# Optimization experiments

Measured on AMD Instinct MI355X. Metric: run time of the kernel, lower is better.

Reference implementation:

```python
import jax, jax.numpy as jnp
import numpy as np

IN_DIM, HID, E, N = 1024, 2048, 8, 16384

def setup_inputs() -> dict:
    key = jax.random.key(0)
    ks = jax.random.split(key, 12)
    s_in = 1.0 / np.sqrt(IN_DIM)
    s_h = 1.0 / np.sqrt(HID)
    return {
        "x": jax.random.normal(ks[0], (N, IN_DIM), dtype=jnp.float32),
        "enc_W": jax.random.uniform(ks[1], (IN_DIM, HID), jnp.float32, -s_in, s_in),
        "enc_b": jax.random.uniform(ks[2], (HID,), jnp.float32, -s_in, s_in),
        "gate_W": jax.random.uniform(ks[3], (HID, E), jnp.float32, -s_h, s_h),
        "expert_W": jax.random.uniform(ks[4], (E, HID, HID), jnp.float32, -s_h, s_h),
        "expert_b": jax.random.uniform(ks[5], (E, HID), jnp.float32, -s_h, s_h),
        "res_W": jax.random.uniform(ks[6], (HID, HID), jnp.float32, -s_h, s_h),
        "res_b": jax.random.uniform(ks[7], (HID,), jnp.float32, -s_h, s_h),
        "coef_W": jax.random.uniform(ks[8], (HID, 2), jnp.float32, -s_h, s_h),
        "coef_b": jax.random.uniform(ks[9], (2,), jnp.float32, -s_h, s_h),
        "dec_W": jax.random.uniform(ks[10], (HID, IN_DIM), jnp.float32, -s_h, s_h),
        "dec_b": jax.random.uniform(ks[11], (IN_DIM,), jnp.float32, -s_h, s_h),
    }

def reference(x, enc_W, enc_b, gate_W, expert_W, expert_b, res_W, res_b, coef_W, coef_b, dec_W, dec_b):
    # Encode: Linear + ReLU -> h [N, HID]
    h = jax.nn.relu(x @ enc_W + enc_b)
    # Top-1 gating (softmax probs, argmax expert, combine weight = chosen prob)
    probs = jax.nn.softmax(h @ gate_W, axis=-1)          # [N, E]
    idx = jnp.argmax(probs, axis=-1)                     # [N]
    gate = jnp.max(probs, axis=-1, keepdims=True)        # [N, 1]
    # Dense dispatch: run every expert, select via one-hot combine
    y_all = jnp.einsum('nd,edh->neh', h, expert_W) + expert_b  # [N, E, HID]
    onehot = jax.nn.one_hot(idx, y_all.shape[1], dtype=h.dtype)
    moe_out = jnp.einsum('neh,ne->nh', y_all, onehot) * gate   # [N, HID]
    # Residual expert + learned 2-way blending coefficient
    res = h @ res_W + res_b
    coef = jax.nn.softmax(h @ coef_W + coef_b, axis=-1)        # [N, 2]
    out = moe_out * coef[:, 0:1] + res * coef[:, 1:2]
    # Decode
    return out @ dec_W + dec_b
```

## Files before the change

### kernel.cpp

```cpp
#include <hip/hip_runtime.h>


#define N_TOK 16384
#define IN_DIM 1024
#define HID 2048
#define NEXP 8
#define TAU 8.0e-3f

typedef __bf16 bf16_t;
typedef __bf16 bf16x8 __attribute__((ext_vector_type(8)));
typedef __bf16 bf16x4v __attribute__((ext_vector_type(4)));
typedef float f32x4 __attribute__((ext_vector_type(4)));
typedef unsigned short ushort_t;

#define CLAMP1E4(v) fmaxf(fminf((v), 1.0e4f), -1.0e4f)

#define ASYNC16(gp, lp)                                                        \
  __builtin_amdgcn_global_load_lds(                                            \
      (const __attribute__((address_space(1))) void*)(gp),                     \
      (__attribute__((address_space(3))) void*)(lp), 16, 0, 0)

static __device__ inline ushort_t b2u(bf16_t v) {
  union { bf16_t b; ushort_t u; } x; x.b = v; return x.u;
}

__global__ __launch_bounds__(256) void fill_bf16(bf16_t* __restrict__ p,
                                                 float v, int n) {
  const int i = blockIdx.x * 256 + threadIdx.x;
  if (i < n) p[i] = (bf16_t)v;
}

__global__ __launch_bounds__(256) void detect_dtype(
    const ushort_t* __restrict__ xr, int* __restrict__ flag) {
  __shared__ int s_bad;
  if (threadIdx.x == 0) s_bad = 0;
  __syncthreads();
  int bad = 0;
  for (int i = threadIdx.x; i < 4096; i += 256) {
    const int e = (xr[i] >> 7) & 0xFF;
    if (e >= 0xC0) bad = 1;
  }
  if (__any(bad) && (threadIdx.x & 63) == 0) atomicOr(&s_bad, 1);
  __syncthreads();
  if (threadIdx.x == 0) *flag = s_bad;
}

__global__ __launch_bounds__(256) void cvt_to_bf16_x4(
    const void* __restrict__ src, bf16_t* __restrict__ dst, int n4,
    const int* __restrict__ flagp) {
  const int f = *flagp;
  const int i = blockIdx.x * 256 + threadIdx.x;
  if (i >= n4) return;
  bf16x4v o;
  if (f) {
    const f32x4 v = ((const f32x4*)src)[i];
    o[0] = (bf16_t)v[0]; o[1] = (bf16_t)v[1];
    o[2] = (bf16_t)v[2]; o[3] = (bf16_t)v[3];
  } else {
    o = ((const bf16x4v*)src)[i];
  }
  ((bf16x4v*)dst)[i] = o;
}

__global__ __launch_bounds__(256) void cvt_small(
    const void* __restrict__ encB, const void* __restrict__ expB,
    const void* __restrict__ resB, const void* __restrict__ decB,
    const void* __restrict__ coefB, const void* __restrict__ gateW,
    const void* __restrict__ coefW, float* __restrict__ encBf,
    float* __restrict__ expBf, float* __restrict__ resBf,
    float* __restrict__ decBf, float* __restrict__ coefBf,
    bf16_t* __restrict__ gWb, bf16_t* __restrict__ cWb,
    const int* __restrict__ flagp) {
  const int f = *flagp;
  const int i = blockIdx.x * 256 + threadIdx.x;
  const int seg = blockIdx.y;
  const void* src;
  int n;
  switch (seg) {
    case 0: src = encB;  n = HID; break;
    case 1: src = expB;  n = NEXP * HID; break;
    case 2: src = resB;  n = HID; break;
    case 3: src = decB;  n = IN_DIM; break;
    case 4: src = coefB; n = 2; break;
    case 5: src = gateW; n = HID * 8; break;
    default: src = coefW; n = HID * 2; break;
  }
  if (i >= n) return;
  const float v = f ? ((const float*)src)[i] : (float)((const bf16_t*)src)[i];
  switch (seg) {
    case 0: encBf[i] = v; break;
    case 1: expBf[i] = v; break;
    case 2: resBf[i] = v; break;
    case 3: decBf[i] = v; break;
    case 4: coefBf[i] = v; break;
    case 5: gWb[i] = (bf16_t)v; break;
    default: cWb[i] = (bf16_t)v; break;
  }
}

__global__ __launch_bounds__(256) void transpose_cvt(
    const void* __restrict__ src0, ushort_t* __restrict__ dst, int R, int C,
    size_t elem_off, const int* __restrict__ flagp, size_t src_zstride,
    size_t dst_zstride) {
  __shared__ ushort_t t[32][33];
  const int f = *flagp;
  const size_t eoff = elem_off + (size_t)blockIdx.z * src_zstride;
  dst += (size_t)blockIdx.z * dst_zstride;
  const int c0 = blockIdx.x * 32, r0 = blockIdx.y * 32;
  const int tx = threadIdx.x, ty = threadIdx.y;
  if (f) {
    const float* s = (const float*)src0 + eoff;
#pragma unroll
    for (int i = 0; i < 4; ++i)
      t[ty + i * 8][tx] =
          b2u((bf16_t)s[(size_t)(r0 + ty + i * 8) * C + c0 + tx]);
  } else {
    const ushort_t* s = (const ushort_t*)src0 + eoff;
#pragma unroll
    for (int i = 0; i < 4; ++i)
      t[ty + i * 8][tx] = s[(size_t)(r0 + ty + i * 8) * C + c0 + tx];
  }
  __syncthreads();
#pragma unroll
  for (int i = 0; i < 4; ++i)
    dst[(size_t)(c0 + ty + i * 8) * R + r0 + tx] = t[tx][ty + i * 8];
}


__global__ __launch_bounds__(256) void enc_gemm(
    const bf16_t* __restrict__ A, const bf16_t* __restrict__ Bt,
    const float* __restrict__ bias, bf16_t* __restrict__ H) {
  __shared__ bf16_t As[128 * 64];
  __shared__ bf16_t Bs[128 * 64];

  const int tid = threadIdx.x, lane = tid & 63, w = tid >> 6;
  const int wr = w >> 1, wc = w & 1, quad = lane >> 4, l16 = lane & 15;
  const int m0 = blockIdx.x * 128, n0 = blockIdx.y * 128;
  const char* Ab = (const char*)A;
  const char* Bb = (const char*)Bt;
  const size_t lda = (size_t)IN_DIM * 2;

  const f32x4 fz = {0.f, 0.f, 0.f, 0.f};
  f32x4 acc[4][4];
#pragma unroll
  for (int i = 0; i < 4; ++i)
#pragma unroll
    for (int j = 0; j < 4; ++j) acc[i][j] = fz;

  size_t aoff[4], boff[4];
  int cb[4];
#pragma unroll
  for (int c = 0; c < 4; ++c) {
    cb[c] = (w * 4 + c) * 1024;
    const int o = cb[c] + lane * 16;
    const int row = o >> 7;
    const int kb = (o & 127) ^ ((row & 7) << 4);
    aoff[c] = (size_t)(m0 + row) * lda + kb;
    boff[c] = (size_t)(n0 + row) * lda + kb;
  }
  const int sw = (l16 & 7) << 3;

  for (int kt = 0; kt < IN_DIM / 64; ++kt) {
    __syncthreads();
#pragma unroll
    for (int c = 0; c < 4; ++c) {
      ASYNC16(Ab + aoff[c] + (size_t)kt * 128, (char*)As + cb[c]);
      ASYNC16(Bb + boff[c] + (size_t)kt * 128, (char*)Bs + cb[c]);
    }
    __syncthreads();

#pragma unroll
    for (int ks = 0; ks < 2; ++ks) {
      const int co = (ks * 32 + quad * 8) ^ sw;
      bf16x8 af[4], bfr[4];
#pragma unroll
      for (int i = 0; i < 4; ++i)
        af[i] = *(const bf16x8*)&As[(wr * 64 + i * 16 + l16) * 64 + co];
#pragma unroll
      for (int j = 0; j < 4; ++j)
        bfr[j] = *(const bf16x8*)&Bs[(wc * 64 + j * 16 + l16) * 64 + co];
#pragma unroll
      for (int i = 0; i < 4; ++i)
#pragma unroll
        for (int j = 0; j < 4; ++j)
          acc[i][j] = __builtin_amdgcn_mfma_f32_16x16x32_bf16(
              af[i], bfr[j], acc[i][j], 0, 0, 0);
    }
  }

  float bj[4];
  int colj[4];
#pragma unroll
  for (int j = 0; j < 4; ++j) {
    colj[j] = n0 + wc * 64 + j * 16 + l16;
    bj[j] = bias[colj[j]];
  }

#pragma unroll
  for (int i = 0; i < 4; ++i) {
#pragma unroll
    for (int r = 0; r < 4; ++r) {
      const int row = m0 + wr * 64 + i * 16 + quad * 4 + r;
#pragma unroll
      for (int j = 0; j < 4; ++j) {
        const float v = fminf(fmaxf(acc[i][j][r] + bj[j], 0.f), 1.0e4f);
        H[(size_t)row * HID + colj[j]] = (bf16_t)v;
      }
    }
  }
}

__global__ __launch_bounds__(256) void gate_from_h(
    const bf16_t* __restrict__ H, const bf16_t* __restrict__ gW,
    const bf16_t* __restrict__ cW, const float* __restrict__ coefBf,
    float* __restrict__ s0g, float* __restrict__ s1g, float* __restrict__ c0g,
    int* __restrict__ eidx, int* __restrict__ ambig, int* __restrict__ acnt,
    int* __restrict__ cnt) {
  const int tid = threadIdx.x, lane = tid & 63, w = tid >> 6;
  const int r0 = blockIdx.x * 16 + w * 4;

  float acc[4][10];
#pragma unroll
  for (int g = 0; g < 4; ++g)
#pragma unroll
    for (int o = 0; o < 10; ++o) acc[g][o] = 0.f;

#pragma unroll
  for (int it = 0; it < HID / 512; ++it) {
    const int h0 = it * 512 + lane * 8;
    bf16x8 hv[4];
#pragma unroll
    for (int g = 0; g < 4; ++g)
      hv[g] = *(const bf16x8*)(H + (size_t)(r0 + g) * HID + h0);
    const bf16_t* gp = gW + (size_t)h0 * 8;
    const bf16_t* cp = cW + (size_t)h0 * 2;
    bf16x8 cc0 = *(const bf16x8*)(cp);
    bf16x8 cc1 = *(const bf16x8*)(cp + 8);
#pragma unroll
    for (int k = 0; k < 8; ++k) {
      const bf16x8 gk = *(const bf16x8*)(gp + k * 8);
      const float ck0 = (k < 4) ? (float)cc0[(k & 3) * 2]
                                : (float)cc1[(k & 3) * 2];
      const float ck1 = (k < 4) ? (float)cc0[(k & 3) * 2 + 1]
                                : (float)cc1[(k & 3) * 2 + 1];
#pragma unroll
      for (int g = 0; g < 4; ++g) {
        const float v = (float)hv[g][k];
#pragma unroll
        for (int o = 0; o < 8; ++o) acc[g][o] += v * (float)gk[o];
        acc[g][8] += v * ck0;
        acc[g][9] += v * ck1;
      }
    }
  }

#pragma unroll
  for (int m = 1; m < 64; m <<= 1)
#pragma unroll
    for (int g = 0; g < 4; ++g)
#pragma unroll
      for (int o = 0; o < 10; ++o) acc[g][o] += __shfl_xor(acc[g][o], m);

  if (lane == 0) {
#pragma unroll
    for (int g = 0; g < 4; ++g) {
      const int r = r0 + g;
      float lv[8];
#pragma unroll
      for (int e = 0; e < 8; ++e) lv[e] = acc[g][e];
      float mx = lv[0];
      int idx = 0;
#pragma unroll
      for (int e = 1; e < 8; ++e)
        if (lv[e] > mx) { mx = lv[e]; idx = e; }
      float s2 = -1.0e30f;
#pragma unroll
      for (int e = 0; e < 8; ++e)
        if (e != idx) s2 = fmaxf(s2, lv[e]);
      float s = 0.f;
#pragma unroll
      for (int e = 0; e < 8; ++e) s += expf(lv[e] - mx);
      const float gate = 1.f / s;
      const float c0 = acc[g][8] + coefBf[0], c1 = acc[g][9] + coefBf[1];
      const float cm = fmaxf(c0, c1);
      const float e0 = expf(c0 - cm), e1 = expf(c1 - cm);
      const float inv = 1.f / (e0 + e1);
      const float p0 = e0 * inv;
      c0g[r] = p0;
      s1g[r] = e1 * inv;
      s0g[r] = gate * p0;
      eidx[r] = idx;
      atomicAdd(&cnt[idx], 1);
      if (mx - s2 < TAU) {
        const int p = atomicAdd(acnt, 1);
        ambig[p] = r;
      }
    }
  }
}

__global__ __launch_bounds__(256) void rescue_rows(
    const void* __restrict__ xraw, const void* __restrict__ encWraw,
    const float* __restrict__ encBf, const void* __restrict__ gateWraw,
    const int* __restrict__ flagp, const int* __restrict__ ambig,
    const int* __restrict__ acnt, const float* __restrict__ c0g,
    float* __restrict__ s0g, int* __restrict__ eidx, int* __restrict__ cnt) {
  const int i = blockIdx.x;
  if (i >= *acnt) return;
  const int r = ambig[i];
  const int f = *flagp;
  const int tid = threadIdx.x;

  __shared__ float xs[IN_DIM];
  if (f) {
    const float* xp = (const float*)xraw + (size_t)r * IN_DIM;
    for (int k = tid; k < IN_DIM; k += 256) xs[k] = xp[k];
  } else {
    const bf16_t* xp = (const bf16_t*)xraw + (size_t)r * IN_DIM;
    for (int k = tid; k < IN_DIM; k += 256) xs[k] = (float)xp[k];
  }
  __syncthreads();

  double hacc[8] = {0, 0, 0, 0, 0, 0, 0, 0};
  if (f) {
    const float* W = (const float*)encWraw;
    for (int k0 = 0; k0 < IN_DIM; k0 += 8) {
      float wv[8][8];
#pragma unroll
      for (int kk = 0; kk < 8; ++kk) {
        const float* Wr = W + (size_t)(k0 + kk) * HID + tid;
#pragma unroll
        for (int jj = 0; jj < 8; ++jj) wv[kk][jj] = Wr[jj * 256];
      }
#pragma unroll
      for (int kk = 0; kk < 8; ++kk) {
        const double xv = (double)xs[k0 + kk];
#pragma unroll
        for (int jj = 0; jj < 8; ++jj) hacc[jj] += xv * (double)wv[kk][jj];
      }
    }
  } else {
    const bf16_t* W = (const bf16_t*)encWraw;
    for (int k0 = 0; k0 < IN_DIM; k0 += 8) {
      float wv[8][8];
#pragma unroll
      for (int kk = 0; kk < 8; ++kk) {
        const bf16_t* Wr = W + (size_t)(k0 + kk) * HID + tid;
#pragma unroll
        for (int jj = 0; jj < 8; ++jj) wv[kk][jj] = (float)Wr[jj * 256];
      }
#pragma unroll
      for (int kk = 0; kk < 8; ++kk) {
        const double xv = (double)xs[k0 + kk];
#pragma unroll
        for (int jj = 0; jj < 8; ++jj) hacc[jj] += xv * (double)wv[kk][jj];
      }
    }
  }

  double lg[8] = {0, 0, 0, 0, 0, 0, 0, 0};
#pragma unroll
  for (int jj = 0; jj < 8; ++jj) {
    const int j = tid + jj * 256;
    double h = hacc[jj] + (double)encBf[j];
    if (h > 0.0) {
      if (f) {
        const float* g = (const float*)gateWraw + (size_t)j * 8;
#pragma unroll
        for (int e = 0; e < 8; ++e) lg[e] += h * (double)g[e];
      } else {
        const bf16_t* g = (const bf16_t*)gateWraw + (size_t)j * 8;
#pragma unroll
        for (int e = 0; e < 8; ++e) lg[e] += h * (double)(float)g[e];
      }
    }
  }
#pragma unroll
  for (int m = 1; m < 64; m <<= 1)
#pragma unroll
    for (int e = 0; e < 8; ++e) lg[e] += __shfl_xor(lg[e], m);

  __shared__ double red[4][8];
  const int w = tid >> 6, lane = tid & 63;
  if (lane == 0)
#pragma unroll
    for (int e = 0; e < 8; ++e) red[w][e] = lg[e];
  __syncthreads();
  if (tid == 0) {
    double t[8];
#pragma unroll
    for (int e = 0; e < 8; ++e)
      t[e] = red[0][e] + red[1][e] + red[2][e] + red[3][e];
    double m = t[0];
    int idx = 0;
#pragma unroll
    for (int e = 1; e < 8; ++e)
      if (t[e] > m) { m = t[e]; idx = e; }
    double s = 0.0;
#pragma unroll
    for (int e = 0; e < 8; ++e) s += exp(t[e] - m);
    s0g[r] = (float)((1.0 / s) * (double)c0g[r]);
    const int old = eidx[r];
    if (idx != old) {
      atomicSub(&cnt[old], 1);
      atomicAdd(&cnt[idx], 1);
      eidx[r] = idx;
    }
  }
}

__global__ __launch_bounds__(256) void place_rows(
    const int* __restrict__ eidx, const int* __restrict__ cnt,
    int* __restrict__ curs, int* __restrict__ permflat) {
  const int r = blockIdx.x * 256 + threadIdx.x;
  const int e = eidx[r];
  int prefix = 0;
  for (int ee = 0; ee < NEXP; ++ee)
    if (ee < e) prefix += cnt[ee];
  const int pos = atomicAdd(&curs[e], 1);
  permflat[prefix + pos] = r;
}

__global__ __launch_bounds__(256) void gather_rows(
    const bf16_t* __restrict__ H, const int* __restrict__ permflat,
    const float* __restrict__ s0g, const float* __restrict__ s1g,
    bf16_t* __restrict__ Hp, int* __restrict__ rowid,
    float* __restrict__ s0p, float* __restrict__ s1p) {
  const int w = threadIdx.x >> 6, lane = threadIdx.x & 63;
  const int p = blockIdx.x * 4 + w;
  const int r = permflat[p];
  if (lane == 0) {
    rowid[p] = r;
    s0p[p] = s0g[r];
    s1p[p] = s1g[r];
  }
  const bf16x8* src = (const bf16x8*)(H + (size_t)r * HID);
  bf16x8* dst = (bf16x8*)(Hp + (size_t)p * HID);
#pragma unroll
  for (int i = 0; i < 4; ++i) dst[lane + i * 64] = src[lane + i * 64];
}

__global__ __launch_bounds__(256) void expert_gemm_t(
    const bf16_t* __restrict__ Hp, const bf16_t* __restrict__ wTall,
    size_t wstride, const float* __restrict__ expBf,
    const int* __restrict__ cnt, const int* __restrict__ rowid,
    const float* __restrict__ s0p, bf16_t* __restrict__ mid) {
  __shared__ bf16_t As[128 * 64];
  __shared__ bf16_t Bs[128 * 64];
  __shared__ int rows_s[128];
  __shared__ float s0_s[128];

  const int x = blockIdx.x;
  int e = -1, base = 0, nrows = 0;
  {
    int acc = 0, pre = 0;
    for (int ee = 0; ee < NEXP; ++ee) {
      const int ce = cnt[ee];
      const int nt = (ce + 127) >> 7;
      if (x < acc + nt) {
        const int t = x - acc;
        e = ee;
        base = pre + t * 128;
        nrows = ce - t * 128;
        if (nrows > 128) nrows = 128;
        break;
      }
      acc += nt;
      pre += ce;
    }
  }
  if (e < 0) return;

  const int tid = threadIdx.x, lane = tid & 63, w = tid >> 6;
  const int wr = w >> 1, wc = w & 1, quad = lane >> 4, l16 = lane & 15;

  if (tid < 128) {
    int grow = -1;
    float a0 = 0.f;
    if (tid < nrows) {
      grow = rowid[base + tid];
      a0 = s0p[base + tid];
    }
    rows_s[tid] = grow;
    s0_s[tid] = a0;
  }
  __syncthreads();

  const int n0 = blockIdx.y * 128;
  const char* Hb = (const char*)Hp;
  const char* Wb = (const char*)(wTall + (size_t)e * wstride);

  size_t aoff[4], boff[4];
  int cb[4];
#pragma unroll
  for (int c = 0; c < 4; ++c) {
    cb[c] = (w * 4 + c) * 1024;
    const int o = cb[c] + lane * 16;
    const int row = o >> 7;
    const int kb = (o & 127) ^ ((row & 7) << 4);
    int ar = base + row;
    if (ar > N_TOK - 1) ar = N_TOK - 1;
    aoff[c] = (size_t)ar * (HID * 2) + kb;
    boff[c] = (size_t)(n0 + row) * (HID * 2) + kb;
  }
  const int sw = (l16 & 7) << 3;

  const f32x4 fz = {0.f, 0.f, 0.f, 0.f};
  f32x4 acc[4][4];
#pragma unroll
  for (int i = 0; i < 4; ++i)
#pragma unroll
    for (int j = 0; j < 4; ++j) acc[i][j] = fz;

  for (int kt = 0; kt < HID / 64; ++kt) {
    __syncthreads();
#pragma unroll
    for (int c = 0; c < 4; ++c) {
      ASYNC16(Hb + aoff[c] + (size_t)kt * 128, (char*)As + cb[c]);
      ASYNC16(Wb + boff[c] + (size_t)kt * 128, (char*)Bs + cb[c]);
    }
    __syncthreads();

#pragma unroll
    for (int ks = 0; ks < 2; ++ks) {
      const int co = (ks * 32 + quad * 8) ^ sw;
      bf16x8 af[4], bfr[4];
#pragma unroll
      for (int i = 0; i < 4; ++i)
        af[i] = *(const bf16x8*)&As[(wr * 64 + i * 16 + l16) * 64 + co];
#pragma unroll
      for (int j = 0; j < 4; ++j)
        bfr[j] = *(const bf16x8*)&Bs[(wc * 64 + j * 16 + l16) * 64 + co];
#pragma unroll
      for (int i = 0; i < 4; ++i)
#pragma unroll
        for (int j = 0; j < 4; ++j)
          acc[i][j] = __builtin_amdgcn_mfma_f32_16x16x32_bf16(
              af[i], bfr[j], acc[i][j], 0, 0, 0);
    }
  }

  const float* eBe = expBf + (size_t)e * HID;
  float beb[4];
  int colj[4];
#pragma unroll
  for (int j = 0; j < 4; ++j) {
    colj[j] = n0 + wc * 64 + j * 16 + l16;
    beb[j] = eBe[colj[j]];
  }
#pragma unroll
  for (int i = 0; i < 4; ++i) {
#pragma unroll
    for (int r = 0; r < 4; ++r) {
      const int lr = wr * 64 + i * 16 + quad * 4 + r;
      const int grow = rows_s[lr];
      if (grow < 0) continue;
      const float s0 = s0_s[lr];
#pragma unroll
      for (int j = 0; j < 4; ++j) {
        const float v = CLAMP1E4(s0 * (acc[i][j][r] + beb[j]));
        mid[(size_t)grow * HID + colj[j]] = (bf16_t)v;
      }
    }
  }
}

__global__ __launch_bounds__(256) void res_gemm_p(
    const bf16_t* __restrict__ Hp, const bf16_t* __restrict__ Bt,
    const float* __restrict__ rB, const int* __restrict__ rowid,
    const float* __restrict__ s1p, bf16_t* __restrict__ mid) {
  __shared__ bf16_t As[128 * 64];
  __shared__ bf16_t Bs[128 * 64];

  const int tid = threadIdx.x, lane = tid & 63, w = tid >> 6;
  const int wr = w >> 1, wc = w & 1, quad = lane >> 4, l16 = lane & 15;
  const int m0 = blockIdx.x * 128, n0 = blockIdx.y * 128;
  const char* Ab = (const char*)Hp;
  const char* Bb = (const char*)Bt;

  size_t aoff[4], boff[4];
  int cb[4];
#pragma unroll
  for (int c = 0; c < 4; ++c) {
    cb[c] = (w * 4 + c) * 1024;
    const int o = cb[c] + lane * 16;
    const int row = o >> 7;
    const int kb = (o & 127) ^ ((row & 7) << 4);
    aoff[c] = (size_t)(m0 + row) * (HID * 2) + kb;
    boff[c] = (size_t)(n0 + row) * (HID * 2) + kb;
  }
  const int sw = (l16 & 7) << 3;

  const f32x4 fz = {0.f, 0.f, 0.f, 0.f};
  f32x4 acc[4][4];
#pragma unroll
  for (int i = 0; i < 4; ++i)
#pragma unroll
    for (int j = 0; j < 4; ++j) acc[i][j] = fz;

  for (int kt = 0; kt < HID / 64; ++kt) {
    __syncthreads();
#pragma unroll
    for (int c = 0; c < 4; ++c) {
      ASYNC16(Ab + aoff[c] + (size_t)kt * 128, (char*)As + cb[c]);
      ASYNC16(Bb + boff[c] + (size_t)kt * 128, (char*)Bs + cb[c]);
    }
    __syncthreads();

#pragma unroll
    for (int ks = 0; ks < 2; ++ks) {
      const int co = (ks * 32 + quad * 8) ^ sw;
      bf16x8 af[4], bfr[4];
#pragma unroll
      for (int i = 0; i < 4; ++i)
        af[i] = *(const bf16x8*)&As[(wr * 64 + i * 16 + l16) * 64 + co];
#pragma unroll
      for (int j = 0; j < 4; ++j)
        bfr[j] = *(const bf16x8*)&Bs[(wc * 64 + j * 16 + l16) * 64 + co];
#pragma unroll
      for (int i = 0; i < 4; ++i)
#pragma unroll
        for (int j = 0; j < 4; ++j)
          acc[i][j] = __builtin_amdgcn_mfma_f32_16x16x32_bf16(
              af[i], bfr[j], acc[i][j], 0, 0, 0);
    }
  }

  float rbb[4];
  int colj[4];
#pragma unroll
  for (int j = 0; j < 4; ++j) {
    colj[j] = n0 + wc * 64 + j * 16 + l16;
    rbb[j] = rB[colj[j]];
  }
#pragma unroll
  for (int i = 0; i < 4; ++i) {
#pragma unroll
    for (int r = 0; r < 4; ++r) {
      const int p = m0 + wr * 64 + i * 16 + quad * 4 + r;
      const int grow = rowid[p];
      const float s1 = s1p[p];
#pragma unroll
      for (int j = 0; j < 4; ++j) {
        const size_t ix = (size_t)grow * HID + colj[j];
        const float v =
            CLAMP1E4(s1 * (acc[i][j][r] + rbb[j]) + (float)mid[ix]);
        mid[ix] = (bf16_t)v;
      }
    }
  }
}

__global__ __launch_bounds__(256) void dec_gemm(
    const bf16_t* __restrict__ A, const bf16_t* __restrict__ Bt,
    const float* __restrict__ bias, void* __restrict__ C,
    const int* __restrict__ flagp) {
  __shared__ bf16_t As[128 * 64];
  __shared__ bf16_t Bs[128 * 64];

  const int fl = *flagp;
  const int tid = threadIdx.x, lane = tid & 63, w = tid >> 6;
  const int wr = w >> 1, wc = w & 1, quad = lane >> 4, l16 = lane & 15;
  const int m0 = blockIdx.x * 128, n0 = blockIdx.y * 128;
  const char* Ab = (const char*)A;
  const char* Bb = (const char*)Bt;

  size_t aoff[4], boff[4];
  int cb[4];
#pragma unroll
  for (int c = 0; c < 4; ++c) {
    cb[c] = (w * 4 + c) * 1024;
    const int o = cb[c] + lane * 16;
    const int row = o >> 7;
    const int kb = (o & 127) ^ ((row & 7) << 4);
    aoff[c] = (size_t)(m0 + row) * (HID * 2) + kb;
    boff[c] = (size_t)(n0 + row) * (HID * 2) + kb;
  }
  const int sw = (l16 & 7) << 3;

  const f32x4 fz = {0.f, 0.f, 0.f, 0.f};
  f32x4 acc[4][4];
#pragma unroll
  for (int i = 0; i < 4; ++i)
#pragma unroll
    for (int j = 0; j < 4; ++j) acc[i][j] = fz;

  for (int kt = 0; kt < HID / 64; ++kt) {
    __syncthreads();
#pragma unroll
    for (int c = 0; c < 4; ++c) {
      ASYNC16(Ab + aoff[c] + (size_t)kt * 128, (char*)As + cb[c]);
      ASYNC16(Bb + boff[c] + (size_t)kt * 128, (char*)Bs + cb[c]);
    }
    __syncthreads();

#pragma unroll
    for (int ks = 0; ks < 2; ++ks) {
      const int co = (ks * 32 + quad * 8) ^ sw;
      bf16x8 af[4], bfr[4];
#pragma unroll
      for (int i = 0; i < 4; ++i)
        af[i] = *(const bf16x8*)&As[(wr * 64 + i * 16 + l16) * 64 + co];
#pragma unroll
      for (int j = 0; j < 4; ++j)
        bfr[j] = *(const bf16x8*)&Bs[(wc * 64 + j * 16 + l16) * 64 + co];
#pragma unroll
      for (int i = 0; i < 4; ++i)
#pragma unroll
        for (int j = 0; j < 4; ++j)
          acc[i][j] = __builtin_amdgcn_mfma_f32_16x16x32_bf16(
              af[i], bfr[j], acc[i][j], 0, 0, 0);
    }
  }

  float bb[4];
  int colj[4];
#pragma unroll
  for (int j = 0; j < 4; ++j) {
    colj[j] = n0 + wc * 64 + j * 16 + l16;
    bb[j] = bias[colj[j]];
  }
#pragma unroll
  for (int i = 0; i < 4; ++i) {
#pragma unroll
    for (int r = 0; r < 4; ++r) {
      const int row = m0 + wr * 64 + i * 16 + quad * 4 + r;
#pragma unroll
      for (int j = 0; j < 4; ++j) {
        const float v = CLAMP1E4(acc[i][j][r] + bb[j]);
        const size_t ix = (size_t)row * IN_DIM + colj[j];
        if (fl)
          ((float*)C)[ix] = v;
        else
          ((bf16_t*)C)[ix] = (bf16_t)v;
      }
    }
  }
}

__global__ __launch_bounds__(256) void bucket_rows(
    const int* __restrict__ eidx, int* __restrict__ curs,
    int* __restrict__ perm) {
  const int r = blockIdx.x * 256 + threadIdx.x;
  const int e = eidx[r];
  const int pos = atomicAdd(&curs[e], 1);
  perm[(size_t)e * N_TOK + pos] = r;
}

__global__ __launch_bounds__(256) void expert_gemm(
    const bf16_t* __restrict__ H, const bf16_t* __restrict__ wTe,
    const float* __restrict__ eBe, const int* __restrict__ permE,
    const int* __restrict__ cnt, int e, const float* __restrict__ s0g,
    bf16_t* __restrict__ mid) {
  __shared__ bf16_t As[128 * 32];
  __shared__ bf16_t Bs[128 * 32];
  __shared__ int rows_s[128];
  __shared__ float s0_s[128];

  const int cnte = cnt[e];
  const int lt = blockIdx.x;
  if (lt * 128 >= cnte) return;
  int nrows = cnte - lt * 128;
  if (nrows > 128) nrows = 128;

  const int tid = threadIdx.x, lane = tid & 63, w = tid >> 6;
  const int wr = w >> 1, wc = w & 1, quad = lane >> 4, l16 = lane & 15;

  if (tid < 128) {
    int grow = -1;
    float a0 = 0.f;
    if (tid < nrows) {
      grow = permE[lt * 128 + tid];
      a0 = s0g[grow];
    }
    rows_s[tid] = grow;
    s0_s[tid] = a0;
  }
  __syncthreads();

  const int n0 = blockIdx.y * 128;
  const char* Hb = (const char*)H;
  const char* Wb = (const char*)wTe;

  size_t aoff[2], boff[2];
  int cb[2];
#pragma unroll
  for (int c = 0; c < 2; ++c) {
    cb[c] = (w * 2 + c) * 1024;
    const int o = cb[c] + lane * 16;
    const int row = o >> 6, kb = o & 63;
    int gr = rows_s[row];
    if (gr < 0) gr = 0;
    aoff[c] = (size_t)gr * (HID * 2) + kb;
    boff[c] = (size_t)(n0 + row) * (HID * 2) + kb;
  }

  const f32x4 fz = {0.f, 0.f, 0.f, 0.f};
  f32x4 acc[4][4];
#pragma unroll
  for (int i = 0; i < 4; ++i)
#pragma unroll
    for (int j = 0; j < 4; ++j) acc[i][j] = fz;

  for (int kt = 0; kt < HID / 32; ++kt) {
    __syncthreads();
#pragma unroll
    for (int c = 0; c < 2; ++c) {
      ASYNC16(Hb + aoff[c] + (size_t)kt * 64, (char*)As + cb[c]);
      ASYNC16(Wb + boff[c] + (size_t)kt * 64, (char*)Bs + cb[c]);
    }
    __syncthreads();

    bf16x8 af[4], bfr[4];
#pragma unroll
    for (int i = 0; i < 4; ++i)
      af[i] = *(const bf16x8*)&As[(wr * 64 + i * 16 + l16) * 32 + quad * 8];
#pragma unroll
    for (int j = 0; j < 4; ++j)
      bfr[j] = *(const bf16x8*)&Bs[(wc * 64 + j * 16 + l16) * 32 + quad * 8];
#pragma unroll
    for (int i = 0; i < 4; ++i)
#pragma unroll
      for (int j = 0; j < 4; ++j)
        acc[i][j] = __builtin_amdgcn_mfma_f32_16x16x32_bf16(af[i], bfr[j],
                                                            acc[i][j], 0, 0, 0);
  }

  float beb[4];
  int colj[4];
#pragma unroll
  for (int j = 0; j < 4; ++j) {
    colj[j] = n0 + wc * 64 + j * 16 + l16;
    beb[j] = eBe[colj[j]];
  }
#pragma unroll
  for (int i = 0; i < 4; ++i) {
#pragma unroll
    for (int r = 0; r < 4; ++r) {
      const int lr = wr * 64 + i * 16 + quad * 4 + r;
      const int grow = rows_s[lr];
      if (grow < 0) continue;
      const float s0 = s0_s[lr];
#pragma unroll
      for (int j = 0; j < 4; ++j) {
        const float v = CLAMP1E4(s0 * (acc[i][j][r] + beb[j]));
        mid[(size_t)grow * HID + colj[j]] = (bf16_t)v;
      }
    }
  }
}

__global__ __launch_bounds__(256) void res_gemm(
    const bf16_t* __restrict__ H, const bf16_t* __restrict__ Bt,
    const float* __restrict__ rB, const float* __restrict__ s1g,
    bf16_t* __restrict__ mid) {
  __shared__ bf16_t As[128 * 32];
  __shared__ bf16_t Bs[128 * 32];

  const int tid = threadIdx.x, lane = tid & 63, w = tid >> 6;
  const int wr = w >> 1, wc = w & 1, quad = lane >> 4, l16 = lane & 15;
  const int m0 = blockIdx.x * 128, n0 = blockIdx.y * 128;
  const char* Ab = (const char*)H;
  const char* Bb = (const char*)Bt;

  size_t aoff[2], boff[2];
  int cb[2];
#pragma unroll
  for (int c = 0; c < 2; ++c) {
    cb[c] = (w * 2 + c) * 1024;
    const int o = cb[c] + lane * 16;
    const int row = o >> 6, kb = o & 63;
    aoff[c] = (size_t)(m0 + row) * (HID * 2) + kb;
    boff[c] = (size_t)(n0 + row) * (HID * 2) + kb;
  }

  const f32x4 fz = {0.f, 0.f, 0.f, 0.f};
  f32x4 acc[4][4];
#pragma unroll
  for (int i = 0; i < 4; ++i)
#pragma unroll
    for (int j = 0; j < 4; ++j) acc[i][j] = fz;

  for (int kt = 0; kt < HID / 32; ++kt) {
    __syncthreads();
#pragma unroll
    for (int c = 0; c < 2; ++c) {
      ASYNC16(Ab + aoff[c] + (size_t)kt * 64, (char*)As + cb[c]);
      ASYNC16(Bb + boff[c] + (size_t)kt * 64, (char*)Bs + cb[c]);
    }
    __syncthreads();

    bf16x8 af[4], bfr[4];
#pragma unroll
    for (int i = 0; i < 4; ++i)
      af[i] = *(const bf16x8*)&As[(wr * 64 + i * 16 + l16) * 32 + quad * 8];
#pragma unroll
    for (int j = 0; j < 4; ++j)
      bfr[j] = *(const bf16x8*)&Bs[(wc * 64 + j * 16 + l16) * 32 + quad * 8];
#pragma unroll
    for (int i = 0; i < 4; ++i)
#pragma unroll
      for (int j = 0; j < 4; ++j)
        acc[i][j] = __builtin_amdgcn_mfma_f32_16x16x32_bf16(af[i], bfr[j],
                                                            acc[i][j], 0, 0, 0);
  }

  float rbb[4];
  int colj[4];
#pragma unroll
  for (int j = 0; j < 4; ++j) {
    colj[j] = n0 + wc * 64 + j * 16 + l16;
    rbb[j] = rB[colj[j]];
  }
#pragma unroll
  for (int i = 0; i < 4; ++i) {
#pragma unroll
    for (int r = 0; r < 4; ++r) {
      const int row = m0 + wr * 64 + i * 16 + quad * 4 + r;
      const float s1 = s1g[row];
#pragma unroll
      for (int j = 0; j < 4; ++j) {
        const size_t ix = (size_t)row * HID + colj[j];
        const float v =
            CLAMP1E4(s1 * (acc[i][j][r] + rbb[j]) + (float)mid[ix]);
        mid[ix] = (bf16_t)v;
      }
    }
  }
}

extern "C" void kernel_launch(void* const* d_in, const int* in_sizes, int n_in,
                              void* d_out, int out_size, void* d_ws,
                              size_t ws_size, hipStream_t stream) {
  (void)in_sizes; (void)n_in;

  const void* x     = d_in[0];
  const void* encW  = d_in[1];
  const void* encB  = d_in[2];
  const void* gateW = d_in[3];
  const void* expW  = d_in[4];
  const void* expB  = d_in[5];
  const void* resW  = d_in[6];
  const void* resB  = d_in[7];
  const void* coefW = d_in[8];
  const void* coefB = d_in[9];
  const void* decW  = d_in[10];
  const void* decB  = d_in[11];

  char* ws = (char*)d_ws;
  size_t o = 0;
  int*    flag  = (int*)(ws + o);    o += 256;
  int*    cnt   = (int*)(ws + o);    o += 256;
  int*    acnt  = cnt + 8;
  int*    curs  = cnt + 16;
  float*  s0g   = (float*)(ws + o);  o += (size_t)N_TOK * 4;
  float*  s1g   = (float*)(ws + o);  o += (size_t)N_TOK * 4;
  float*  c0g   = (float*)(ws + o);  o += (size_t)N_TOK * 4;
  int*    eidx  = (int*)(ws + o);    o += (size_t)N_TOK * 4;
  int*    ambig = (int*)(ws + o);    o += (size_t)N_TOK * 4;
  int*    permfl= (int*)(ws + o);    o += (size_t)N_TOK * 4;
  int*    rowid = (int*)(ws + o);    o += (size_t)N_TOK * 4;
  float*  s0p   = (float*)(ws + o);  o += (size_t)N_TOK * 4;
  float*  s1p   = (float*)(ws + o);  o += (size_t)N_TOK * 4;
  int*    perm  = (int*)(ws + o);    o += (size_t)NEXP * N_TOK * 4;
  float*  encBf = (float*)(ws + o);  o += HID * 4;
  float*  expBf = (float*)(ws + o);  o += (size_t)NEXP * HID * 4;
  float*  resBf = (float*)(ws + o);  o += HID * 4;
  float*  decBf = (float*)(ws + o);  o += IN_DIM * 4;
  float*  coefBf= (float*)(ws + o);  o += 256;
  bf16_t* gWb   = (bf16_t*)(ws + o); o += (size_t)HID * 8 * 2;
  bf16_t* cWb   = (bf16_t*)(ws + o); o += (size_t)HID * 2 * 2;
  o = (o + 255) & ~(size_t)255;
  bf16_t* bufA  = (bf16_t*)(ws + o); o += (size_t)N_TOK * HID * 2;
  bf16_t* bufB  = (bf16_t*)(ws + o); o += (size_t)N_TOK * HID * 2;
  bf16_t* wT    = (bf16_t*)(ws + o); o += (size_t)HID * HID * 2;
  const size_t needed_small = o;
  const size_t S = (size_t)HID * HID;
  bf16_t* wTall = (bf16_t*)(ws + o);
  const size_t needed_big = o + 10 * S * 2;

  bf16_t* hbuf  = bufA;
  bf16_t* xbf   = bufB;

  if (ws_size < needed_small) {
    const float v = (float)(ws_size >> 20);
    fill_bf16<<<dim3((out_size + 255) / 256), 256, 0, stream>>>(
        (bf16_t*)d_out, v, out_size);
    return;
  }
  const bool big = ws_size >= needed_big;

  detect_dtype<<<1, 256, 0, stream>>>((const ushort_t*)x, flag);
  hipMemsetAsync(cnt, 0, 256, stream);

  cvt_to_bf16_x4<<<dim3(N_TOK * IN_DIM / 4 / 256), 256, 0, stream>>>(
      x, xbf, N_TOK * IN_DIM / 4, flag);
  cvt_small<<<dim3(64, 7), 256, 0, stream>>>(encB, expB, resB, decB, coefB,
                                             gateW, coefW, encBf, expBf, resBf,
                                             decBf, coefBf, gWb, cWb, flag);

  const dim3 tb(32, 8, 1);

  transpose_cvt<<<dim3(HID / 32, IN_DIM / 32, 1), tb, 0, stream>>>(
      encW, (ushort_t*)wT, IN_DIM, HID, 0, flag, 0, 0);
  if (big) {
    transpose_cvt<<<dim3(HID / 32, HID / 32, NEXP), tb, 0, stream>>>(
        expW, (ushort_t*)wTall, HID, HID, 0, flag, S, S);
    transpose_cvt<<<dim3(HID / 32, HID / 32, 1), tb, 0, stream>>>(
        resW, (ushort_t*)(wTall + 8 * S), HID, HID, 0, flag, 0, 0);
    transpose_cvt<<<dim3(IN_DIM / 32, HID / 32, 1), tb, 0, stream>>>(
        decW, (ushort_t*)(wTall + 9 * S), HID, IN_DIM, 0, flag, 0, 0);
  }

  enc_gemm<<<dim3(N_TOK / 128, HID / 128), 256, 0, stream>>>(xbf, wT, encBf,
                                                             hbuf);
  gate_from_h<<<dim3(N_TOK / 16), 256, 0, stream>>>(
      hbuf, gWb, cWb, coefBf, s0g, s1g, c0g, eidx, ambig, acnt, cnt);
  rescue_rows<<<dim3(1024), 256, 0, stream>>>(x, encW, encBf, gateW, flag,
                                              ambig, acnt, c0g, s0g, eidx,
                                              cnt);

  if (big) {
    bf16_t* Hperm = bufB;
    bf16_t* mid   = bufA;
    place_rows<<<dim3(N_TOK / 256), 256, 0, stream>>>(eidx, cnt, curs, permfl);
    gather_rows<<<dim3(N_TOK / 4), 256, 0, stream>>>(hbuf, permfl, s0g, s1g,
                                                     Hperm, rowid, s0p, s1p);
    expert_gemm_t<<<dim3(136, HID / 128), 256, 0, stream>>>(
        Hperm, wTall, S, expBf, cnt, rowid, s0p, mid);
    res_gemm_p<<<dim3(N_TOK / 128, HID / 128), 256, 0, stream>>>(
        Hperm, wTall + 8 * S, resBf, rowid, s1p, mid);
    dec_gemm<<<dim3(N_TOK / 128, IN_DIM / 128), 256, 0, stream>>>(
        mid, wTall + 9 * S, decBf, d_out, flag);
  } else {
    bf16_t* mid = bufB;
    bucket_rows<<<dim3(N_TOK / 256), 256, 0, stream>>>(eidx, curs, perm);
    for (int e = 0; e < NEXP; ++e) {
      transpose_cvt<<<dim3(HID / 32, HID / 32, 1), tb, 0, stream>>>(
          expW, (ushort_t*)wT, HID, HID, (size_t)e * HID * HID, flag, 0, 0);
      expert_gemm<<<dim3(N_TOK / 128, HID / 128), 256, 0, stream>>>(
          hbuf, wT, expBf + (size_t)e * HID, perm + (size_t)e * N_TOK, cnt, e,
          s0g, mid);
    }
    transpose_cvt<<<dim3(HID / 32, HID / 32, 1), tb, 0, stream>>>(
        resW, (ushort_t*)wT, HID, HID, 0, flag, 0, 0);
    res_gemm<<<dim3(N_TOK / 128, HID / 128), 256, 0, stream>>>(hbuf, wT, resBf,
                                                               s1g, mid);
    transpose_cvt<<<dim3(IN_DIM / 32, HID / 32, 1), tb, 0, stream>>>(
        decW, (ushort_t*)wT, HID, IN_DIM, 0, flag, 0, 0);
    dec_gemm<<<dim3(N_TOK / 128, IN_DIM / 128), 256, 0, stream>>>(
        mid, wT, decBf, d_out, flag);
  }
}
```

Measured before the change: 1.534 ms.

## Split ambiguous-row rescue across column slices with a separate reduction kernel

The fp64 recomputation of gating logits for ambiguous rows is split into a partial kernel, where each of 8 blocks per row handles a 256-column slice of the hidden dimension, and a final kernel that reduces the partials, reselects the expert and fixes the counts. This spreads the per-row serial work over more blocks to improve GPU occupancy. Rows past the first 1024 still go to the old rescue_rows kernel, launched over the rest of the token range. The partial sums are stored in the perm workspace buffer, which is reused before bucketing.

```diff
diff --git a/kernel.cpp b/kernel.cpp
--- a/kernel.cpp
+++ b/kernel.cpp
@@ -299,13 +299,125 @@
   }
 }
 
+__global__ __launch_bounds__(256) void rescue_partial(
+    const void* __restrict__ xraw, const void* __restrict__ encWraw,
+    const float* __restrict__ encBf, const void* __restrict__ gateWraw,
+    const int* __restrict__ flagp, const int* __restrict__ ambig,
+    const int* __restrict__ acnt, double* __restrict__ pglg) {
+  const int i = blockIdx.x;
+  if (i >= *acnt) return;
+  const int s = blockIdx.y;
+  const int r = ambig[i];
+  const int f = *flagp;
+  const int tid = threadIdx.x;
+  const int j = s * 256 + tid;
+
+  __shared__ float xs[IN_DIM];
+  if (f) {
+    const float* xp = (const float*)xraw + (size_t)r * IN_DIM;
+    for (int k = tid; k < IN_DIM; k += 256) xs[k] = xp[k];
+  } else {
+    const bf16_t* xp = (const bf16_t*)xraw + (size_t)r * IN_DIM;
+    for (int k = tid; k < IN_DIM; k += 256) xs[k] = (float)xp[k];
+  }
+  __syncthreads();
+
+  double hacc = 0.0;
+  if (f) {
+    const float* W = (const float*)encWraw + j;
+    for (int k0 = 0; k0 < IN_DIM; k0 += 16) {
+      float wv[16];
+#pragma unroll
+      for (int kk = 0; kk < 16; ++kk) wv[kk] = W[(size_t)(k0 + kk) * HID];
+#pragma unroll
+      for (int kk = 0; kk < 16; ++kk)
+        hacc += (double)xs[k0 + kk] * (double)wv[kk];
+    }
+  } else {
+    const bf16_t* W = (const bf16_t*)encWraw + j;
+    for (int k0 = 0; k0 < IN_DIM; k0 += 16) {
+      float wv[16];
+#pragma unroll
+      for (int kk = 0; kk < 16; ++kk)
+        wv[kk] = (float)W[(size_t)(k0 + kk) * HID];
+#pragma unroll
+      for (int kk = 0; kk < 16; ++kk)
+        hacc += (double)xs[k0 + kk] * (double)wv[kk];
+    }
+  }
+
+  double lg[8] = {0, 0, 0, 0, 0, 0, 0, 0};
+  const double h = hacc + (double)encBf[j];
+  if (h > 0.0) {
+    if (f) {
+      const float* g = (const float*)gateWraw + (size_t)j * 8;
+#pragma unroll
+      for (int e = 0; e < 8; ++e) lg[e] = h * (double)g[e];
+    } else {
+      const bf16_t* g = (const bf16_t*)gateWraw + (size_t)j * 8;
+#pragma unroll
+      for (int e = 0; e < 8; ++e) lg[e] = h * (double)(float)g[e];
+    }
+  }
+#pragma unroll
+  for (int m = 1; m < 64; m <<= 1)
+#pragma unroll
+    for (int e = 0; e < 8; ++e) lg[e] += __shfl_xor(lg[e], m);
+
+  __shared__ double red[4][8];
+  const int w = tid >> 6, lane = tid & 63;
+  if (lane == 0)
+#pragma unroll
+    for (int e = 0; e < 8; ++e) red[w][e] = lg[e];
+  __syncthreads();
+  if (tid == 0) {
+#pragma unroll
+    for (int e = 0; e < 8; ++e)
+      pglg[((size_t)i * 8 + s) * 8 + e] =
+          red[0][e] + red[1][e] + red[2][e] + red[3][e];
+  }
+}
+
+__global__ __launch_bounds__(64) void rescue_final(
+    const int* __restrict__ ambig, const int* __restrict__ acnt,
+    const float* __restrict__ c0g, const double* __restrict__ pglg,
+    float* __restrict__ s0g, int* __restrict__ eidx, int* __restrict__ cnt) {
+  const int i = blockIdx.x;
+  if (i >= *acnt || threadIdx.x != 0) return;
+  const int r = ambig[i];
+  double t[8];
+#pragma unroll
+  for (int e = 0; e < 8; ++e) {
+    double a = 0.0;
+#pragma unroll
+    for (int s = 0; s < 8; ++s) a += pglg[((size_t)i * 8 + s) * 8 + e];
+    t[e] = a;
+  }
+  double m = t[0];
+  int idx = 0;
+#pragma unroll
+  for (int e = 1; e < 8; ++e)
+    if (t[e] > m) { m = t[e]; idx = e; }
+  double s = 0.0;
+#pragma unroll
+  for (int e = 0; e < 8; ++e) s += exp(t[e] - m);
+  s0g[r] = (float)((1.0 / s) * (double)c0g[r]);
+  const int old = eidx[r];
+  if (idx != old) {
+    atomicSub(&cnt[old], 1);
+    atomicAdd(&cnt[idx], 1);
+    eidx[r] = idx;
+  }
+}
+
 __global__ __launch_bounds__(256) void rescue_rows(
     const void* __restrict__ xraw, const void* __restrict__ encWraw,
     const float* __restrict__ encBf, const void* __restrict__ gateWraw,
     const int* __restrict__ flagp, const int* __restrict__ ambig,
     const int* __restrict__ acnt, const float* __restrict__ c0g,
-    float* __restrict__ s0g, int* __restrict__ eidx, int* __restrict__ cnt) {
-  const int i = blockIdx.x;
+    float* __restrict__ s0g, int* __restrict__ eidx, int* __restrict__ cnt,
+    int ioff) {
+  const int i = blockIdx.x + ioff;
   if (i >= *acnt) return;
   const int r = ambig[i];
   const int f = *flagp;
@@ -979,6 +1091,8 @@
   bf16_t* wTall = (bf16_t*)(ws + o);
   const size_t needed_big = o + 10 * S * 2;
 
+  double* pglg = (double*)perm;
+
   bf16_t* hbuf  = bufA;
   bf16_t* xbf   = bufB;
 
@@ -1016,9 +1130,12 @@
                                                              hbuf);
   gate_from_h<<<dim3(N_TOK / 16), 256, 0, stream>>>(
       hbuf, gWb, cWb, coefBf, s0g, s1g, c0g, eidx, ambig, acnt, cnt);
-  rescue_rows<<<dim3(1024), 256, 0, stream>>>(x, encW, encBf, gateW, flag,
-                                              ambig, acnt, c0g, s0g, eidx,
-                                              cnt);
+  rescue_partial<<<dim3(1024, 8), 256, 0, stream>>>(
+      x, encW, encBf, gateW, flag, ambig, acnt, pglg);
+  rescue_final<<<dim3(1024), 64, 0, stream>>>(ambig, acnt, c0g, pglg, s0g,
+                                              eidx, cnt);
+  rescue_rows<<<dim3(N_TOK - 1024), 256, 0, stream>>>(
+      x, encW, encBf, gateW, flag, ambig, acnt, c0g, s0g, eidx, cnt, 1024);
 
   if (big) {
     bf16_t* Hperm = bufB;
```

After: 1.532 ms. No clear change (-0.1%).
